# Performance work log

Measured on AMD Instinct MI355X. Metric: run time of the kernel, lower is better.

Reference implementation:

```python
import jax, jax.numpy as jnp
import numpy as np
import math

D = 2048  # hidden_size
B, S = 4, 2048
EPS = 1e-5


def _ln(z, g, b):
    m = jnp.mean(z, axis=-1, keepdims=True)
    v = jnp.mean(jnp.square(z - m), axis=-1, keepdims=True)
    return (z - m) * jax.lax.rsqrt(v + EPS) * g + b


def _rotate_half(x):
    h = x.shape[-1] // 2
    return jnp.concatenate([-x[..., h:], x[..., :h]], axis=-1)


def _mas_normalize(logits):
    m = jnp.max(jnp.abs(logits), axis=-1, keepdims=True)
    return logits / (m + 1e-9)


def setup_inputs() -> dict:
    key = jax.random.key(0)
    ks = jax.random.split(key, 12)
    std = 0.02
    return {
        "x": jax.random.normal(ks[0], (B, S, D), dtype=jnp.float32),
        "position_ids": jnp.arange(S, dtype=jnp.int32),
        "ln1_g": jnp.ones((D,), jnp.float32),
        "ln1_b": jnp.zeros((D,), jnp.float32),
        # stacked params for [q, k, v, o]
        "mu_w": std * jax.random.normal(ks[1], (4, D, D), dtype=jnp.float32),
        "mu_b": jnp.zeros((4, D), jnp.float32),
        "proto_w": std * jax.random.normal(ks[2], (4, D, D), dtype=jnp.float32),
        "gate": jnp.zeros((4, D), jnp.float32),
        "pt_w": std * jax.random.normal(ks[3], (4, D, D), dtype=jnp.float32),
        "pln_g": jnp.ones((4, D), jnp.float32),
        "pln_b": jnp.zeros((4, D), jnp.float32),
        "incoming": std * jax.random.normal(ks[4], (4, D, D), dtype=jnp.float32),
    }


def reference(x, position_ids, ln1_g, ln1_b, mu_w, mu_b, proto_w, gate,
              pt_w, pln_g, pln_b, incoming):
    d = x.shape[-1]
    inv_sqrt_d = 1.0 / math.sqrt(d)

    # proto_state = proto_weight + LN(Linear(incoming))  per module [4, D, D]
    prc = jnp.einsum('nij,noj->nio', incoming, pt_w)
    proto_state = proto_w + _ln(prc, pln_g[:, None, :], pln_b[:, None, :])

    ln1_out = _ln(x, ln1_g, ln1_b)            # [B,S,D]
    ctx = jnp.mean(ln1_out, axis=1)           # [B,D]

    # qkv computation outputs: silu(ln1_out @ mu_w.T + mu_b) for n in {q,k,v}
    comp = jax.nn.silu(jnp.einsum('bsd,nod->nbso', ln1_out, mu_w[:3])
                       + mu_b[:3][:, None, None, :])            # [3,B,S,D]
    # routing from context vector
    match_ctx = jnp.einsum('bd,nod->nbo', ctx, proto_state[:3]) * inv_sqrt_d
    routing = match_ctx + gate[:3][:, None, :]                  # [3,B,D]
    gating = _mas_normalize(routing)
    masked = gating[:, :, None, :] * comp                       # [3,B,S,D]
    q, k, v = masked[0], masked[1], masked[2]

    # RoPE over full hidden dim (num_heads == 1)
    seq = position_ids.shape[0]
    inv_freq = 1.0 / (10000.0 ** (jnp.arange(0, d, 2, dtype=jnp.float32) / d))
    t = jnp.arange(seq, dtype=jnp.float32)
    freqs = t[:, None] * inv_freq[None, :]
    emb = jnp.concatenate([freqs, freqs], axis=-1)              # [S,D]
    cos = jnp.cos(emb)[position_ids]
    sin = jnp.sin(emb)[position_ids]
    q = q * cos + _rotate_half(q) * sin
    k = k * cos + _rotate_half(k) * sin

    # causal single-head attention, scale 1/sqrt(head_dim=D)
    scores = jnp.einsum('bqd,bkd->bqk', q, k) * inv_sqrt_d      # [B,S,S]
    causal = jnp.tril(jnp.ones((seq, seq), dtype=bool))
    scores = jnp.where(causal, scores, jnp.finfo(scores.dtype).min)
    probs = jax.nn.softmax(scores, axis=-1)
    attn_out = jnp.einsum('bqk,bkd->bqd', probs, v)             # [B,S,D]

    # output SPL + routing
    ctx_o = jnp.mean(attn_out, axis=1)
    c_o = jax.nn.silu(jnp.einsum('bsd,od->bso', attn_out, mu_w[3]) + mu_b[3])
    match_o = jnp.einsum('bd,od->bo', ctx_o, proto_state[3]) * inv_sqrt_d
    gating_o = _mas_normalize(match_o + gate[3])
    x_out = x + gating_o[:, None, :] * c_o
    return x_out
```

## Files before the change

kernel.cpp:

```cpp
#include <hip/hip_runtime.h>
#include <hip/hip_bf16.h>

#define Dh 2048
#define Bh 4
#define Sh 2048
#define NROW 8192
#define HALF 1024
#define INV_SQRT_D 0.022097086912079608f
#define LNEPS 1e-5f

typedef __hip_bfloat16 bf16;
typedef short short8 __attribute__((ext_vector_type(8)));
typedef float f32x4 __attribute__((ext_vector_type(4)));

__device__ inline float warp_sum(float x) {
#pragma unroll
  for (int o = 32; o > 0; o >>= 1) x += __shfl_down(x, o);
  return x;
}
__device__ inline float warp_max(float x) {
#pragma unroll
  for (int o = 32; o > 0; o >>= 1) x = fmaxf(x, __shfl_down(x, o));
  return x;
}
__device__ inline float block_sum(float x, float* sm4) {
  x = warp_sum(x);
  int w = threadIdx.x >> 6;
  if ((threadIdx.x & 63) == 0) sm4[w] = x;
  __syncthreads();
  float r = sm4[0] + sm4[1] + sm4[2] + sm4[3];
  __syncthreads();
  return r;
}
__device__ inline float block_max(float x, float* sm4) {
  x = warp_max(x);
  int w = threadIdx.x >> 6;
  if ((threadIdx.x & 63) == 0) sm4[w] = x;
  __syncthreads();
  float r = fmaxf(fmaxf(sm4[0], sm4[1]), fmaxf(sm4[2], sm4[3]));
  __syncthreads();
  return r;
}

__device__ inline void gload_lds16(const void* g, void* lds) {
  __builtin_amdgcn_global_load_lds(
      (const __attribute__((address_space(1))) unsigned int*)(unsigned long long)g,
      (__attribute__((address_space(3))) unsigned int*)(unsigned long long)lds,
      16, 0, 0);
}

template <int MODE>
__global__ __launch_bounds__(512) void pgemm(
    const bf16* __restrict__ Aall, const bf16* __restrict__ Ball,
    void* __restrict__ Call, int N, int K, int lda, int ldb,
    long sAz, long sBz, long sCz,
    const float* __restrict__ e0, const float* __restrict__ e1,
    const float* __restrict__ e2) {
  const int bm0 = blockIdx.x * 256;
  const int bn0 = blockIdx.y * 256;
  if (MODE == 2 && bn0 > bm0 + 255) return;
  const int z = blockIdx.z;
  const bf16* A = Aall + (long)z * sAz;
  const bf16* B = Ball + (long)z * sBz;

  __shared__ __align__(16) char smem[65536];
  const int tid = threadIdx.x;
  const int l = tid & 63, w = tid >> 6;
  const int wr = w >> 2, wc = w & 3;

  f32x4 acc[8][4] = {};

  const int nt = (MODE == 3) ? ((bm0 + 256) >> 5) : (K >> 5);

  const int sg = (((l & 3) ^ ((l >> 3) & 3)) << 3);

  auto stageA = [&](int tt, int half) {
    char* dst = smem + ((tt & 1) << 15) + (half << 13) + (w << 10);
    int row = (half << 7) + (w << 4) + (l >> 2);
    gload_lds16(A + (long)(bm0 + row) * lda + (tt << 5) + sg, dst);
  };
  auto stageB = [&](int tt, int half) {
    char* dst = smem + ((tt & 1) << 15) + 16384 + (half << 13) + (w << 10);
    int row = (half << 7) + (w << 4) + (l >> 2);
    gload_lds16(B + (long)(bn0 + row) * ldb + (tt << 5) + sg, dst);
  };

  stageA(0, 0); stageA(0, 1); stageB(0, 0); stageB(0, 1);
  if (nt > 1) { stageB(1, 0); stageB(1, 1); }
  if (nt > 1) asm volatile("s_waitcnt vmcnt(2)" ::: "memory");
  else        asm volatile("s_waitcnt vmcnt(0)" ::: "memory");
  __builtin_amdgcn_sched_barrier(0);
  asm volatile("s_barrier" ::: "memory");

#define PH(FR0, FR1, STG)                                                     \
  do {                                                                        \
    short8 xa0 = *(const short8*)(Ab + abyte + FR0 * 1024);                   \
    short8 xa1 = *(const short8*)(Ab + abyte + FR1 * 1024);                   \
    STG;                                                                      \
    __builtin_amdgcn_s_setprio(1);                                            \
    acc[FR0][0] = __builtin_amdgcn_mfma_f32_16x16x32_bf16(xa0, bfv0, acc[FR0][0], 0, 0, 0); \
    acc[FR1][0] = __builtin_amdgcn_mfma_f32_16x16x32_bf16(xa1, bfv0, acc[FR1][0], 0, 0, 0); \
    acc[FR0][1] = __builtin_amdgcn_mfma_f32_16x16x32_bf16(xa0, bfv1, acc[FR0][1], 0, 0, 0); \
    acc[FR1][1] = __builtin_amdgcn_mfma_f32_16x16x32_bf16(xa1, bfv1, acc[FR1][1], 0, 0, 0); \
    acc[FR0][2] = __builtin_amdgcn_mfma_f32_16x16x32_bf16(xa0, bfv2, acc[FR0][2], 0, 0, 0); \
    acc[FR1][2] = __builtin_amdgcn_mfma_f32_16x16x32_bf16(xa1, bfv2, acc[FR1][2], 0, 0, 0); \
    acc[FR0][3] = __builtin_amdgcn_mfma_f32_16x16x32_bf16(xa0, bfv3, acc[FR0][3], 0, 0, 0); \
    acc[FR1][3] = __builtin_amdgcn_mfma_f32_16x16x32_bf16(xa1, bfv3, acc[FR1][3], 0, 0, 0); \
    __builtin_amdgcn_s_setprio(0);                                            \
  } while (0)

  const int rslot = (((l >> 4) ^ ((l >> 1) & 3)) << 4);

  for (int t = 0; t < nt; ++t) {
    const char* Ab = smem + ((t & 1) << 15);
    const char* Bb = Ab + 16384;
    const int abyte = (((wr << 7) + (l & 15)) << 6) + rslot;
    const int bbyte = (((wc << 6) + (l & 15)) << 6) + rslot;

    short8 bfv0 = *(const short8*)(Bb + bbyte + 0 * 1024);
    short8 bfv1 = *(const short8*)(Bb + bbyte + 1 * 1024);
    short8 bfv2 = *(const short8*)(Bb + bbyte + 2 * 1024);
    short8 bfv3 = *(const short8*)(Bb + bbyte + 3 * 1024);

    PH(0, 1, if (t + 1 < nt) stageA(t + 1, 0));
    PH(2, 3, if (t + 1 < nt) stageA(t + 1, 1));
    asm volatile("s_barrier" ::: "memory");
    PH(4, 5, if (t + 2 < nt) stageB(t + 2, 0));
    PH(6, 7, if (t + 2 < nt) stageB(t + 2, 1));
    if (t < nt - 1) {
      if (t + 2 < nt) asm volatile("s_waitcnt vmcnt(2)" ::: "memory");
      else            asm volatile("s_waitcnt vmcnt(0)" ::: "memory");
      __builtin_amdgcn_sched_barrier(0);
      asm volatile("s_barrier" ::: "memory");
    }
  }
#undef PH

  const int lc = l & 15, lr4 = (l >> 4) << 2;
#pragma unroll
  for (int fr = 0; fr < 8; ++fr) {
    int gr0 = bm0 + (wr << 7) + fr * 16 + lr4;
#pragma unroll
    for (int fc = 0; fc < 4; ++fc) {
      int gc = bn0 + (wc << 6) + fc * 16 + lc;
#pragma unroll
      for (int qv = 0; qv < 4; ++qv) {
        int gr = gr0 + qv;
        float a = acc[fr][fc][qv];
        if (MODE == 0) {
          ((float*)Call + (long)z * sCz)[(long)gr * N + gc] = a;
        } else if (MODE == 1) {
          float val = a + e0[z * Dh + gc];
          float sil = val / (1.f + __expf(-val));
          int bb = gr >> 11;
          float g = e1[(z * Bh + bb) * Dh + gc];
          ((bf16*)Call + (long)z * sCz)[(long)gr * N + gc] =
              __float2bfloat16(sil * g);
        } else if (MODE == 2) {
          ((float*)Call + (long)z * sCz)[(long)gr * N + gc] = a * INV_SQRT_D;
        } else if (MODE == 3) {
          ((bf16*)Call + (long)z * sCz)[(long)gr * N + gc] = __float2bfloat16(a);
        } else {
          float val = a + e0[gc];
          float sil = val / (1.f + __expf(-val));
          int bb = gr >> 11;
          ((float*)Call)[(long)gr * N + gc] =
              e2[(long)gr * N + gc] + e1[bb * Dh + gc] * sil;
        }
      }
    }
  }
}

__global__ __launch_bounds__(256) void cvt3_kernel(
    const float* __restrict__ s0, const float* __restrict__ s1,
    const float* __restrict__ s2, bf16* __restrict__ o0, bf16* __restrict__ o1,
    bf16* __restrict__ o2, long n) {
  const float* in = (blockIdx.y == 0) ? s0 : (blockIdx.y == 1) ? s1 : s2;
  bf16* out = (blockIdx.y == 0) ? o0 : (blockIdx.y == 1) ? o1 : o2;
  long i = ((long)blockIdx.x * 256 + threadIdx.x) * 4;
  if (i >= n) return;
  float4 v = *(const float4*)(in + i);
  out[i + 0] = __float2bfloat16(v.x);
  out[i + 1] = __float2bfloat16(v.y);
  out[i + 2] = __float2bfloat16(v.z);
  out[i + 3] = __float2bfloat16(v.w);
}

__global__ __launch_bounds__(256) void transpose_kernel(const bf16* __restrict__ in,
                                                        bf16* __restrict__ out) {
  __shared__ bf16 t[64][65];
  int b = blockIdx.z;
  int s0 = blockIdx.x * 64, d0 = blockIdx.y * 64;
  const bf16* ib = in + (long)b * Sh * Dh;
  bf16* ob = out + (long)b * Sh * Dh;
  int tx = threadIdx.x & 63, ty = threadIdx.x >> 6;
#pragma unroll
  for (int r = ty; r < 64; r += 4) t[r][tx] = ib[(long)(s0 + r) * Dh + d0 + tx];
  __syncthreads();
#pragma unroll
  for (int r = ty; r < 64; r += 4) ob[(long)(d0 + r) * Sh + s0 + tx] = t[tx][r];
}

__global__ __launch_bounds__(256) void ln1_kernel(const float* __restrict__ x,
    const float* __restrict__ g, const float* __restrict__ b, bf16* __restrict__ out) {
  __shared__ float sm4[4];
  long r = blockIdx.x;
  const float* row = x + r * Dh;
  float v[8];
  float s = 0.f, s2 = 0.f;
#pragma unroll
  for (int c = 0; c < 8; ++c) {
    float t = row[threadIdx.x + c * 256];
    v[c] = t; s += t; s2 += t * t;
  }
  s = block_sum(s, sm4);
  s2 = block_sum(s2, sm4);
  float mean = s * (1.f / Dh);
  float rstd = rsqrtf(s2 * (1.f / Dh) - mean * mean + LNEPS);
#pragma unroll
  for (int c = 0; c < 8; ++c) {
    int o = threadIdx.x + c * 256;
    out[r * Dh + o] = __float2bfloat16((v[c] - mean) * rstd * g[o] + b[o]);
  }
}

__global__ __launch_bounds__(256) void meanrow_kernel(const bf16* __restrict__ in,
                                                      float* __restrict__ outbd) {
  int gid = blockIdx.x * 256 + threadIdx.x;
  int s0 = blockIdx.y * 128;
  long base = ((long)(gid >> 11) * Sh + s0) * Dh + (gid & 2047);
  float s = 0.f;
  for (int t = 0; t < 128; ++t) s += __bfloat162float(in[base + (long)t * Dh]);
  atomicAdd(&outbd[gid], s * (1.f / Sh));
}

__global__ __launch_bounds__(256) void route_kernel(
    const float* __restrict__ prc, const float* __restrict__ proto_w,
    const float* __restrict__ pln_g, const float* __restrict__ pln_b,
    const float* __restrict__ gate, const float* __restrict__ ctx,
    float* __restrict__ routing, float* __restrict__ ps3) {
  __shared__ float sm4[4];
  int i = blockIdx.x, n = blockIdx.y;
  long rb = ((long)n * Dh + i) * Dh;
  float v[8];
  float s = 0.f, s2 = 0.f;
#pragma unroll
  for (int c = 0; c < 8; ++c) {
    float t = prc[rb + threadIdx.x + c * 256];
    v[c] = t; s += t; s2 += t * t;
  }
  s = block_sum(s, sm4);
  s2 = block_sum(s2, sm4);
  float mean = s * (1.f / Dh);
  float rstd = rsqrtf(s2 * (1.f / Dh) - mean * mean + LNEPS);
  if (n == 3) {
#pragma unroll
    for (int c = 0; c < 8; ++c) {
      int o = threadIdx.x + c * 256;
      float ps = proto_w[rb + o] + (v[c] - mean) * rstd * pln_g[3 * Dh + o] + pln_b[3 * Dh + o];
      ps3[(long)i * Dh + o] = ps;
    }
  } else {
    float acc[4] = {0.f, 0.f, 0.f, 0.f};
#pragma unroll
    for (int c = 0; c < 8; ++c) {
      int o = threadIdx.x + c * 256;
      float ps = proto_w[rb + o] + (v[c] - mean) * rstd * pln_g[n * Dh + o] + pln_b[n * Dh + o];
#pragma unroll
      for (int b = 0; b < 4; ++b) acc[b] += ps * ctx[b * Dh + o];
    }
    for (int b = 0; b < 4; ++b) {
      float r = block_sum(acc[b], sm4);
      if (threadIdx.x == 0)
        routing[(n * 4 + b) * Dh + i] = r * INV_SQRT_D + gate[n * Dh + i];
    }
  }
}

__global__ __launch_bounds__(256) void route_o_kernel(
    const float* __restrict__ ps3, const float* __restrict__ ctxo,
    const float* __restrict__ gate, float* __restrict__ routing) {
  __shared__ float sm4[4];
  int i = blockIdx.x;
  float acc[4] = {0.f, 0.f, 0.f, 0.f};
#pragma unroll
  for (int c = 0; c < 8; ++c) {
    int o = threadIdx.x + c * 256;
    float p = ps3[(long)i * Dh + o];
#pragma unroll
    for (int b = 0; b < 4; ++b) acc[b] += p * ctxo[b * Dh + o];
  }
  for (int b = 0; b < 4; ++b) {
    float r = block_sum(acc[b], sm4);
    if (threadIdx.x == 0)
      routing[(12 + b) * Dh + i] = r * INV_SQRT_D + gate[3 * Dh + i];
  }
}

__global__ __launch_bounds__(256) void masnorm_kernel(const float* __restrict__ rin,
                                                      float* __restrict__ gout) {
  __shared__ float sm4[4];
  long r = blockIdx.x;
  float m = 0.f;
#pragma unroll
  for (int c = 0; c < 8; ++c)
    m = fmaxf(m, fabsf(rin[r * Dh + threadIdx.x + c * 256]));
  m = block_max(m, sm4);
  float inv = 1.f / (m + 1e-9f);
#pragma unroll
  for (int c = 0; c < 8; ++c) {
    int o = threadIdx.x + c * 256;
    gout[r * Dh + o] = rin[r * Dh + o] * inv;
  }
}

__global__ __launch_bounds__(256) void rope_table_kernel(float* __restrict__ cosT,
                                                         float* __restrict__ sinT) {
  int idx = blockIdx.x * 256 + threadIdx.x;
  int t = idx >> 10, f = idx & 1023;
  float inv_freq = expf(-(float)f * (9.210340371976184f / 1024.f));
  float ang = (float)t * inv_freq;
  cosT[idx] = cosf(ang);
  sinT[idx] = sinf(ang);
}

__global__ __launch_bounds__(256) void rope_kernel(bf16* __restrict__ q, bf16* __restrict__ k,
    const int* __restrict__ pos, const float* __restrict__ cosT,
    const float* __restrict__ sinT) {
  long r = blockIdx.x;
  int s = (int)(r & (Sh - 1));
  int p = pos[s];
#pragma unroll
  for (int c = 0; c < 4; ++c) {
    int t = threadIdx.x + c * 256;
    float cv = cosT[(long)p * HALF + t];
    float sv = sinT[(long)p * HALF + t];
    long i1 = r * Dh + t, i2 = i1 + HALF;
    float q1 = __bfloat162float(q[i1]), q2 = __bfloat162float(q[i2]);
    q[i1] = __float2bfloat16(q1 * cv - q2 * sv);
    q[i2] = __float2bfloat16(q2 * cv + q1 * sv);
    float k1 = __bfloat162float(k[i1]), k2 = __bfloat162float(k[i2]);
    k[i1] = __float2bfloat16(k1 * cv - k2 * sv);
    k[i2] = __float2bfloat16(k2 * cv + k1 * sv);
  }
}

__global__ __launch_bounds__(256) void softmax_kernel(const float* __restrict__ scores,
                                                      bf16* __restrict__ probs) {
  __shared__ float buf[Sh];
  __shared__ float sm4[4];
  long r = blockIdx.x;
  int qi = (int)(r & (Sh - 1));
  const float* row = scores + r * (long)Sh;
  bf16* prow = probs + r * (long)Sh;
  int n = qi + 1;
  float m = -3.0e38f;
  for (int o = threadIdx.x; o < n; o += 256) {
    float x = row[o]; buf[o] = x; m = fmaxf(m, x);
  }
  m = block_max(m, sm4);
  float s = 0.f;
  for (int o = threadIdx.x; o < n; o += 256) {
    float e = __expf(buf[o] - m); buf[o] = e; s += e;
  }
  s = block_sum(s, sm4);
  float inv = 1.f / s;
  for (int o = threadIdx.x; o < n; o += 256) prow[o] = __float2bfloat16(buf[o] * inv);
  for (int o = n + (int)threadIdx.x; o < Sh; o += 256) prow[o] = __float2bfloat16(0.f);
}

extern "C" void kernel_launch(void* const* d_in, const int* in_sizes, int n_in,
                              void* d_out, int out_size, void* d_ws, size_t ws_size,
                              hipStream_t stream) {
  const float* x       = (const float*)d_in[0];
  const int*   pos     = (const int*)d_in[1];
  const float* ln1_g   = (const float*)d_in[2];
  const float* ln1_b   = (const float*)d_in[3];
  const float* mu_w    = (const float*)d_in[4];
  const float* mu_b    = (const float*)d_in[5];
  const float* proto_w = (const float*)d_in[6];
  const float* gate    = (const float*)d_in[7];
  const float* pt_w    = (const float*)d_in[8];
  const float* pln_g   = (const float*)d_in[9];
  const float* pln_b   = (const float*)d_in[10];
  const float* incoming= (const float*)d_in[11];

  char* w = (char*)d_ws;
  const long BF = 33554432L;
  bf16*  ln1    = (bf16*)(w);
  bf16*  qb     = (bf16*)(w + BF);
  bf16*  kb     = (bf16*)(w + 2 * BF);
  bf16*  vb     = (bf16*)(w + 3 * BF);
  bf16*  attn   = (bf16*)(w + 4 * BF);
  bf16*  mu_wb  = (bf16*)(w + 5 * BF);
  bf16*  ptw_b  = (bf16*)(w + 6 * BF);
  bf16*  vT     = ptw_b;
  bf16*  inc_b  = (bf16*)(w + 7 * BF);
  bf16*  probs  = inc_b;
  float* ps3    = (float*)(w + 8 * BF);
  float* cosT   = (float*)(w + 8 * BF + 16777216L);
  float* sinT   = cosT + (long)Sh * HALF;
  float* ctx    = sinT + (long)Sh * HALF;
  float* ctxo   = ctx + Bh * Dh;
  float* routing= ctxo + Bh * Dh;
  float* gating = routing + 16 * Dh;
  float* scores = (float*)d_out;

  const long DD4 = 4L * Dh * Dh;

  hipMemsetAsync(ctx, 0, 2L * Bh * Dh * sizeof(float), stream);

  rope_table_kernel<<<(Sh * HALF) / 256, 256, 0, stream>>>(cosT, sinT);
  cvt3_kernel<<<dim3(DD4 / 1024, 3), 256, 0, stream>>>(
      mu_w, incoming, pt_w, mu_wb, inc_b, ptw_b, DD4);
  ln1_kernel<<<NROW, 256, 0, stream>>>(x, ln1_g, ln1_b, ln1);
  meanrow_kernel<<<dim3(32, 16), 256, 0, stream>>>(ln1, ctx);
  pgemm<0><<<dim3(8, 8, 4), 512, 0, stream>>>(
      inc_b, ptw_b, scores, Dh, Dh, Dh, Dh,
      (long)Dh * Dh, (long)Dh * Dh, (long)Dh * Dh, nullptr, nullptr, nullptr);
  route_kernel<<<dim3(Dh, 4), 256, 0, stream>>>(scores, proto_w, pln_g, pln_b,
                                                gate, ctx, routing, ps3);
  masnorm_kernel<<<12, 256, 0, stream>>>(routing, gating);
  pgemm<1><<<dim3(32, 8, 3), 512, 0, stream>>>(
      ln1, mu_wb, qb, Dh, Dh, Dh, Dh,
      0L, (long)Dh * Dh, (long)NROW * Dh, mu_b, gating, nullptr);
  rope_kernel<<<NROW, 256, 0, stream>>>(qb, kb, pos, cosT, sinT);
  pgemm<2><<<dim3(8, 8, 4), 512, 0, stream>>>(
      qb, kb, scores, Sh, Dh, Dh, Dh,
      (long)Sh * Dh, (long)Sh * Dh, (long)Sh * Sh, nullptr, nullptr, nullptr);
  softmax_kernel<<<Bh * Sh, 256, 0, stream>>>(scores, probs);
  transpose_kernel<<<dim3(32, 32, 4), 256, 0, stream>>>(vb, vT);
  pgemm<3><<<dim3(8, 8, 4), 512, 0, stream>>>(
      probs, vT, attn, Dh, Sh, Sh, Sh,
      (long)Sh * Sh, (long)Dh * Sh, (long)Sh * Dh, nullptr, nullptr, nullptr);
  meanrow_kernel<<<dim3(32, 16), 256, 0, stream>>>(attn, ctxo);
  route_o_kernel<<<Dh, 256, 0, stream>>>(ps3, ctxo, gate, routing);
  masnorm_kernel<<<4, 256, 0, stream>>>(routing + 12 * Dh, gating + 12 * Dh);
  pgemm<4><<<dim3(32, 8, 1), 512, 0, stream>>>(
      attn, mu_wb + 3L * Dh * Dh, d_out, Dh, Dh, Dh, Dh,
      0L, 0L, 0L, mu_b + 3 * Dh, gating + 12 * Dh, x);
}
```

Measured before the change: 704.6 us.

## Triple-buffer GEMM LDS stages and remap workgroups across XCDs

The GEMM moves from a 2-stage to a 3-stage LDS ring, prefetching both A and B tiles two iterations ahead. This removes the mid-iteration barrier and gives global loads more time in flight. Workgroup IDs are also remapped so consecutive tiles land on the same XCD, which should improve L2 reuse. LDS use rises to 96KB per block, which may limit occupancy, and the remap assumes the workgroup count divides evenly by 8.

```diff
diff --git a/kernel.cpp b/kernel.cpp
--- a/kernel.cpp
+++ b/kernel.cpp
@@ -56,14 +56,22 @@
     long sAz, long sBz, long sCz,
     const float* __restrict__ e0, const float* __restrict__ e1,
     const float* __restrict__ e2) {
-  const int bm0 = blockIdx.x * 256;
-  const int bn0 = blockIdx.y * 256;
+  const int gx = gridDim.x, gy = gridDim.y;
+  const int nwg = gx * gy * gridDim.z;
+  const int fid = blockIdx.x + gx * (blockIdx.y + gy * blockIdx.z);
+  const int cpx = nwg >> 3;
+  const int wk = (fid & 7) * cpx + (fid >> 3);
+  const int mx = wk % gx;
+  const int rest = wk / gx;
+  const int my = rest % gy;
+  const int bm0 = mx * 256;
+  const int bn0 = my * 256;
   if (MODE == 2 && bn0 > bm0 + 255) return;
-  const int z = blockIdx.z;
+  const int z = rest / gy;
   const bf16* A = Aall + (long)z * sAz;
   const bf16* B = Ball + (long)z * sBz;
 
-  __shared__ __align__(16) char smem[65536];
+  __shared__ __align__(16) char smem[98304];
   const int tid = threadIdx.x;
   const int l = tid & 63, w = tid >> 6;
   const int wr = w >> 2, wc = w & 3;
@@ -75,19 +83,19 @@
   const int sg = (((l & 3) ^ ((l >> 3) & 3)) << 3);
 
   auto stageA = [&](int tt, int half) {
-    char* dst = smem + ((tt & 1) << 15) + (half << 13) + (w << 10);
+    char* dst = smem + (tt % 3) * 16384 + (half << 13) + (w << 10);
     int row = (half << 7) + (w << 4) + (l >> 2);
     gload_lds16(A + (long)(bm0 + row) * lda + (tt << 5) + sg, dst);
   };
   auto stageB = [&](int tt, int half) {
-    char* dst = smem + ((tt & 1) << 15) + 16384 + (half << 13) + (w << 10);
+    char* dst = smem + 49152 + (tt % 3) * 16384 + (half << 13) + (w << 10);
     int row = (half << 7) + (w << 4) + (l >> 2);
     gload_lds16(B + (long)(bn0 + row) * ldb + (tt << 5) + sg, dst);
   };
 
   stageA(0, 0); stageA(0, 1); stageB(0, 0); stageB(0, 1);
-  if (nt > 1) { stageB(1, 0); stageB(1, 1); }
-  if (nt > 1) asm volatile("s_waitcnt vmcnt(2)" ::: "memory");
+  if (nt > 1) { stageA(1, 0); stageA(1, 1); stageB(1, 0); stageB(1, 1); }
+  if (nt > 1) asm volatile("s_waitcnt vmcnt(4)" ::: "memory");
   else        asm volatile("s_waitcnt vmcnt(0)" ::: "memory");
   __builtin_amdgcn_sched_barrier(0);
   asm volatile("s_barrier" ::: "memory");
@@ -112,8 +120,8 @@
   const int rslot = (((l >> 4) ^ ((l >> 1) & 3)) << 4);
 
   for (int t = 0; t < nt; ++t) {
-    const char* Ab = smem + ((t & 1) << 15);
-    const char* Bb = Ab + 16384;
+    const char* Ab = smem + (t % 3) * 16384;
+    const char* Bb = smem + 49152 + (t % 3) * 16384;
     const int abyte = (((wr << 7) + (l & 15)) << 6) + rslot;
     const int bbyte = (((wc << 6) + (l & 15)) << 6) + rslot;
 
@@ -122,13 +130,12 @@
     short8 bfv2 = *(const short8*)(Bb + bbyte + 2 * 1024);
     short8 bfv3 = *(const short8*)(Bb + bbyte + 3 * 1024);
 
-    PH(0, 1, if (t + 1 < nt) stageA(t + 1, 0));
-    PH(2, 3, if (t + 1 < nt) stageA(t + 1, 1));
-    asm volatile("s_barrier" ::: "memory");
-    PH(4, 5, if (t + 2 < nt) stageB(t + 2, 0));
-    PH(6, 7, if (t + 2 < nt) stageB(t + 2, 1));
+    PH(0, 1, if (t + 2 < nt) { stageA(t + 2, 0); stageB(t + 2, 0); });
+    PH(2, 3, if (t + 2 < nt) { stageA(t + 2, 1); stageB(t + 2, 1); });
+    PH(4, 5, );
+    PH(6, 7, );
     if (t < nt - 1) {
-      if (t + 2 < nt) asm volatile("s_waitcnt vmcnt(2)" ::: "memory");
+      if (t + 2 < nt) asm volatile("s_waitcnt vmcnt(4)" ::: "memory");
       else            asm volatile("s_waitcnt vmcnt(0)" ::: "memory");
       __builtin_amdgcn_sched_barrier(0);
       asm volatile("s_barrier" ::: "memory");
```

Result: no change. 710.8 us (+0.9%).

## Add load-balanced 128-row causal PV GEMM and restructure pgemm LDS reads

Applied to the files above, without the earlier changes.

Replaces the causal probs×V GEMM (previously pgemm MODE 3 with 256x256 tiles, whose work varies with the row block) with a dedicated kernel using 128x256 tiles. Block IDs are paired so short and long causal row blocks (mi and 15-mi) are scheduled together, balancing work across CUs and raising block count. The generic pgemm main loop is also rewritten: staging addresses are hoisted out of the loop, A fragments are loaded four at a time instead of two per phase, and explicit lgkmcnt waits are added before barriers. These waits could reduce overlap of LDS reads with MFMA.

```diff
diff --git a/kernel.cpp b/kernel.cpp
--- a/kernel.cpp
+++ b/kernel.cpp
@@ -48,6 +48,12 @@
       (__attribute__((address_space(3))) unsigned int*)(unsigned long long)lds,
       16, 0, 0);
 }
+
+#define MM(R, AF)                                                              \
+  acc[R][0] = __builtin_amdgcn_mfma_f32_16x16x32_bf16(AF, b0, acc[R][0], 0, 0, 0); \
+  acc[R][1] = __builtin_amdgcn_mfma_f32_16x16x32_bf16(AF, b1, acc[R][1], 0, 0, 0); \
+  acc[R][2] = __builtin_amdgcn_mfma_f32_16x16x32_bf16(AF, b2, acc[R][2], 0, 0, 0); \
+  acc[R][3] = __builtin_amdgcn_mfma_f32_16x16x32_bf16(AF, b3, acc[R][3], 0, 0, 0);
 
 template <int MODE>
 __global__ __launch_bounds__(512) void pgemm(
@@ -69,72 +75,68 @@
   const int wr = w >> 2, wc = w & 3;
 
   f32x4 acc[8][4] = {};
-
-  const int nt = (MODE == 3) ? ((bm0 + 256) >> 5) : (K >> 5);
+  const int nt = K >> 5;
 
   const int sg = (((l & 3) ^ ((l >> 3) & 3)) << 3);
-
-  auto stageA = [&](int tt, int half) {
-    char* dst = smem + ((tt & 1) << 15) + (half << 13) + (w << 10);
-    int row = (half << 7) + (w << 4) + (l >> 2);
-    gload_lds16(A + (long)(bm0 + row) * lda + (tt << 5) + sg, dst);
+  const int srow = (w << 4) + (l >> 2);
+  const bf16* aS0 = A + (long)(bm0 + srow) * lda + sg;
+  const bf16* aS1 = A + (long)(bm0 + 128 + srow) * lda + sg;
+  const bf16* bS0 = B + (long)(bn0 + srow) * ldb + sg;
+  const bf16* bS1 = B + (long)(bn0 + 128 + srow) * ldb + sg;
+  char* const dA = smem + (w << 10);
+  char* const dB = smem + 16384 + (w << 10);
+
+  auto stageA = [&](int tt) {
+    int boff = (tt & 1) << 15;
+    gload_lds16(aS0 + (tt << 5), dA + boff);
+    gload_lds16(aS1 + (tt << 5), dA + boff + 8192);
   };
-  auto stageB = [&](int tt, int half) {
-    char* dst = smem + ((tt & 1) << 15) + 16384 + (half << 13) + (w << 10);
-    int row = (half << 7) + (w << 4) + (l >> 2);
-    gload_lds16(B + (long)(bn0 + row) * ldb + (tt << 5) + sg, dst);
+  auto stageB = [&](int tt) {
+    int boff = (tt & 1) << 15;
+    gload_lds16(bS0 + (tt << 5), dB + boff);
+    gload_lds16(bS1 + (tt << 5), dB + boff + 8192);
   };
 
-  stageA(0, 0); stageA(0, 1); stageB(0, 0); stageB(0, 1);
-  if (nt > 1) { stageB(1, 0); stageB(1, 1); }
+  stageA(0); stageB(0);
+  if (nt > 1) stageB(1);
   if (nt > 1) asm volatile("s_waitcnt vmcnt(2)" ::: "memory");
   else        asm volatile("s_waitcnt vmcnt(0)" ::: "memory");
   __builtin_amdgcn_sched_barrier(0);
   asm volatile("s_barrier" ::: "memory");
 
-#define PH(FR0, FR1, STG)                                                     \
-  do {                                                                        \
-    short8 xa0 = *(const short8*)(Ab + abyte + FR0 * 1024);                   \
-    short8 xa1 = *(const short8*)(Ab + abyte + FR1 * 1024);                   \
-    STG;                                                                      \
-    __builtin_amdgcn_s_setprio(1);                                            \
-    acc[FR0][0] = __builtin_amdgcn_mfma_f32_16x16x32_bf16(xa0, bfv0, acc[FR0][0], 0, 0, 0); \
-    acc[FR1][0] = __builtin_amdgcn_mfma_f32_16x16x32_bf16(xa1, bfv0, acc[FR1][0], 0, 0, 0); \
-    acc[FR0][1] = __builtin_amdgcn_mfma_f32_16x16x32_bf16(xa0, bfv1, acc[FR0][1], 0, 0, 0); \
-    acc[FR1][1] = __builtin_amdgcn_mfma_f32_16x16x32_bf16(xa1, bfv1, acc[FR1][1], 0, 0, 0); \
-    acc[FR0][2] = __builtin_amdgcn_mfma_f32_16x16x32_bf16(xa0, bfv2, acc[FR0][2], 0, 0, 0); \
-    acc[FR1][2] = __builtin_amdgcn_mfma_f32_16x16x32_bf16(xa1, bfv2, acc[FR1][2], 0, 0, 0); \
-    acc[FR0][3] = __builtin_amdgcn_mfma_f32_16x16x32_bf16(xa0, bfv3, acc[FR0][3], 0, 0, 0); \
-    acc[FR1][3] = __builtin_amdgcn_mfma_f32_16x16x32_bf16(xa1, bfv3, acc[FR1][3], 0, 0, 0); \
-    __builtin_amdgcn_s_setprio(0);                                            \
-  } while (0)
-
   const int rslot = (((l >> 4) ^ ((l >> 1) & 3)) << 4);
+  const int abyte = (((wr << 7) + (l & 15)) << 6) + rslot;
+  const int bbyte = (((wc << 6) + (l & 15)) << 6) + rslot;
 
   for (int t = 0; t < nt; ++t) {
     const char* Ab = smem + ((t & 1) << 15);
     const char* Bb = Ab + 16384;
-    const int abyte = (((wr << 7) + (l & 15)) << 6) + rslot;
-    const int bbyte = (((wc << 6) + (l & 15)) << 6) + rslot;
-
-    short8 bfv0 = *(const short8*)(Bb + bbyte + 0 * 1024);
-    short8 bfv1 = *(const short8*)(Bb + bbyte + 1 * 1024);
-    short8 bfv2 = *(const short8*)(Bb + bbyte + 2 * 1024);
-    short8 bfv3 = *(const short8*)(Bb + bbyte + 3 * 1024);
-
-    PH(0, 1, if (t + 1 < nt) stageA(t + 1, 0));
-    PH(2, 3, if (t + 1 < nt) stageA(t + 1, 1));
+    short8 b0 = *(const short8*)(Bb + bbyte);
+    short8 b1 = *(const short8*)(Bb + bbyte + 1024);
+    short8 b2 = *(const short8*)(Bb + bbyte + 2048);
+    short8 b3 = *(const short8*)(Bb + bbyte + 3072);
+    short8 a0 = *(const short8*)(Ab + abyte);
+    short8 a1 = *(const short8*)(Ab + abyte + 1024);
+    short8 a2 = *(const short8*)(Ab + abyte + 2048);
+    short8 a3 = *(const short8*)(Ab + abyte + 3072);
+    if (t + 1 < nt) stageA(t + 1);
+    MM(0, a0) MM(1, a1) MM(2, a2) MM(3, a3)
+    asm volatile("s_waitcnt lgkmcnt(0)" ::: "memory");
     asm volatile("s_barrier" ::: "memory");
-    PH(4, 5, if (t + 2 < nt) stageB(t + 2, 0));
-    PH(6, 7, if (t + 2 < nt) stageB(t + 2, 1));
+    short8 a4 = *(const short8*)(Ab + abyte + 4096);
+    short8 a5 = *(const short8*)(Ab + abyte + 5120);
+    short8 a6 = *(const short8*)(Ab + abyte + 6144);
+    short8 a7 = *(const short8*)(Ab + abyte + 7168);
+    if (t + 2 < nt) stageB(t + 2);
+    MM(4, a4) MM(5, a5) MM(6, a6) MM(7, a7)
     if (t < nt - 1) {
+      asm volatile("s_waitcnt lgkmcnt(0)" ::: "memory");
       if (t + 2 < nt) asm volatile("s_waitcnt vmcnt(2)" ::: "memory");
       else            asm volatile("s_waitcnt vmcnt(0)" ::: "memory");
       __builtin_amdgcn_sched_barrier(0);
       asm volatile("s_barrier" ::: "memory");
     }
   }
-#undef PH
 
   const int lc = l & 15, lr4 = (l >> 4) << 2;
 #pragma unroll
@@ -158,8 +160,6 @@
               __float2bfloat16(sil * g);
         } else if (MODE == 2) {
           ((float*)Call + (long)z * sCz)[(long)gr * N + gc] = a * INV_SQRT_D;
-        } else if (MODE == 3) {
-          ((bf16*)Call + (long)z * sCz)[(long)gr * N + gc] = __float2bfloat16(a);
         } else {
           float val = a + e0[gc];
           float sil = val / (1.f + __expf(-val));
@@ -167,6 +167,96 @@
           ((float*)Call)[(long)gr * N + gc] =
               e2[(long)gr * N + gc] + e1[bb * Dh + gc] * sil;
         }
+      }
+    }
+  }
+}
+
+__global__ __launch_bounds__(512) void pgemm_h(
+    const bf16* __restrict__ Aall, const bf16* __restrict__ Ball,
+    bf16* __restrict__ Call, int N, int lda, int ldb,
+    long sAz, long sBz, long sCz) {
+  const int fid = blockIdx.x;
+  const int p = fid >> 8, q = fid & 255;
+  const int mh = q >> 5;
+  const int z = (q >> 3) & 3, ni = q & 7;
+  const int mi = p ? (15 - mh) : mh;
+  const int bm0 = mi * 128, bn0 = ni * 256;
+  const bf16* A = Aall + (long)z * sAz;
+  const bf16* B = Ball + (long)z * sBz;
+
+  __shared__ __align__(16) char smem[49152];
+  const int tid = threadIdx.x;
+  const int l = tid & 63, w = tid >> 6;
+  const int wr = w >> 2, wc = w & 3;
+  f32x4 acc[4][4] = {};
+  const int nt = (bm0 + 128) >> 5;
+
+  const int sg = (((l & 3) ^ ((l >> 3) & 3)) << 3);
+  const int srow = (w << 4) + (l >> 2);
+  const bf16* aS = A + (long)(bm0 + srow) * lda + sg;
+  const bf16* bS0 = B + (long)(bn0 + srow) * ldb + sg;
+  const bf16* bS1 = B + (long)(bn0 + 128 + srow) * ldb + sg;
+  char* const dA = smem + (w << 10);
+  char* const dB = smem + 8192 + (w << 10);
+
+  auto stageA = [&](int tt) {
+    gload_lds16(aS + (tt << 5), dA + (tt & 1) * 24576);
+  };
+  auto stageB = [&](int tt) {
+    int boff = (tt & 1) * 24576;
+    gload_lds16(bS0 + (tt << 5), dB + boff);
+    gload_lds16(bS1 + (tt << 5), dB + boff + 8192);
+  };
+
+  stageA(0); stageB(0);
+  if (nt > 1) stageB(1);
+  if (nt > 1) asm volatile("s_waitcnt vmcnt(2)" ::: "memory");
+  else        asm volatile("s_waitcnt vmcnt(0)" ::: "memory");
+  __builtin_amdgcn_sched_barrier(0);
+  asm volatile("s_barrier" ::: "memory");
+
+  const int rslot = (((l >> 4) ^ ((l >> 1) & 3)) << 4);
+  const int abyte = (((wr << 6) + (l & 15)) << 6) + rslot;
+  const int bbyte = (((wc << 6) + (l & 15)) << 6) + rslot;
+
+  for (int t = 0; t < nt; ++t) {
+    const char* Ab = smem + (t & 1) * 24576;
+    const char* Bb = Ab + 8192;
+    short8 b0 = *(const short8*)(Bb + bbyte);
+    short8 b1 = *(const short8*)(Bb + bbyte + 1024);
+    short8 b2 = *(const short8*)(Bb + bbyte + 2048);
+    short8 b3 = *(const short8*)(Bb + bbyte + 3072);
+    short8 a0 = *(const short8*)(Ab + abyte);
+    short8 a1 = *(const short8*)(Ab + abyte + 1024);
+    if (t + 1 < nt) stageA(t + 1);
+    MM(0, a0) MM(1, a1)
+    asm volatile("s_waitcnt lgkmcnt(0)" ::: "memory");
+    asm volatile("s_barrier" ::: "memory");
+    short8 a2 = *(const short8*)(Ab + abyte + 2048);
+    short8 a3 = *(const short8*)(Ab + abyte + 3072);
+    if (t + 2 < nt) stageB(t + 2);
+    MM(2, a2) MM(3, a3)
+    if (t < nt - 1) {
+      asm volatile("s_waitcnt lgkmcnt(0)" ::: "memory");
+      if (t + 2 < nt) asm volatile("s_waitcnt vmcnt(2)" ::: "memory");
+      else            asm volatile("s_waitcnt vmcnt(0)" ::: "memory");
+      __builtin_amdgcn_sched_barrier(0);
+      asm volatile("s_barrier" ::: "memory");
+    }
+  }
+
+  const int lc = l & 15, lr4 = (l >> 4) << 2;
+  bf16* C = Call + (long)z * sCz;
+#pragma unroll
+  for (int fr = 0; fr < 4; ++fr) {
+    int gr0 = bm0 + (wr << 6) + fr * 16 + lr4;
+#pragma unroll
+    for (int fc = 0; fc < 4; ++fc) {
+      int gc = bn0 + (wc << 6) + fc * 16 + lc;
+#pragma unroll
+      for (int qv = 0; qv < 4; ++qv) {
+        C[(long)(gr0 + qv) * N + gc] = __float2bfloat16(acc[fr][fc][qv]);
       }
     }
   }
@@ -431,9 +521,9 @@
       (long)Sh * Dh, (long)Sh * Dh, (long)Sh * Sh, nullptr, nullptr, nullptr);
   softmax_kernel<<<Bh * Sh, 256, 0, stream>>>(scores, probs);
   transpose_kernel<<<dim3(32, 32, 4), 256, 0, stream>>>(vb, vT);
-  pgemm<3><<<dim3(8, 8, 4), 512, 0, stream>>>(
-      probs, vT, attn, Dh, Sh, Sh, Sh,
-      (long)Sh * Sh, (long)Dh * Sh, (long)Sh * Dh, nullptr, nullptr, nullptr);
+  pgemm_h<<<512, 512, 0, stream>>>(
+      probs, vT, attn, Dh, Sh, Sh,
+      (long)Sh * Sh, (long)Dh * Sh, (long)Sh * Dh);
   meanrow_kernel<<<dim3(32, 16), 256, 0, stream>>>(attn, ctxo);
   route_o_kernel<<<Dh, 256, 0, stream>>>(ps3, ctxo, gate, routing);
   masnorm_kernel<<<4, 256, 0, stream>>>(routing + 12 * Dh, gating + 12 * Dh);
```

After: 678.2 us. 1.04x faster.
